# Kernel tuning notes

Measured on AMD Instinct MI355X. Metric: run time of the kernel, lower is better.

## Reference

```python
import jax, jax.numpy as jnp
import numpy as np

B, C, H, W = 2, 512, 64, 64
G = 32          # GroupNorm groups
EPS = 1e-6


def setup_inputs() -> dict:
    key = jax.random.key(0)
    ks = jax.random.split(key, 10)
    s = 1.0 / np.sqrt(C)
    return {
        "x": jax.random.normal(ks[0], (B, C, H, W), dtype=jnp.float32),
        "gn_w": jnp.ones((C,), jnp.float32),
        "gn_b": jnp.zeros((C,), jnp.float32),
        "wq": jax.random.normal(ks[1], (C, C), jnp.float32) * s,
        "bq": jnp.zeros((C,), jnp.float32),
        "wk": jax.random.normal(ks[2], (C, C), jnp.float32) * s,
        "bk": jnp.zeros((C,), jnp.float32),
        "wv": jax.random.normal(ks[3], (C, C), jnp.float32) * s,
        "bv": jnp.zeros((C,), jnp.float32),
        "wo": jax.random.normal(ks[4], (C, C), jnp.float32) * s,
        "bo": jnp.zeros((C,), jnp.float32),
    }


def reference(x, gn_w, gn_b, wq, bq, wk, bk, wv, bv, wo, bo):
    b, c, h, w = x.shape
    n = h * w
    # GroupNorm(32, eps=1e-6, affine)
    xg = x.reshape(b, G, c // G, h, w)
    mu = xg.mean(axis=(2, 3, 4), keepdims=True)
    var = ((xg - mu) ** 2).mean(axis=(2, 3, 4), keepdims=True)
    hn = ((xg - mu) * jax.lax.rsqrt(var + EPS)).reshape(b, c, h, w)
    hn = hn * gn_w[None, :, None, None] + gn_b[None, :, None, None]
    # 1x1 convs == per-pixel linear over channels; tokens: b n c
    hf = hn.reshape(b, c, n)
    q = jnp.einsum('oc,bcn->bno', wq, hf) + bq  # [b, n, c]
    k = jnp.einsum('oc,bcn->bno', wk, hf) + bk
    v = jnp.einsum('oc,bcn->bno', wv, hf) + bv
    scale = jnp.asarray(c, x.dtype) ** -0.5
    att = jax.nn.softmax(jnp.einsum('bic,bjc->bij', q, k) * scale, axis=-1)
    o = jnp.einsum('bij,bjc->bic', att, v)      # [b, n, c]
    out = jnp.einsum('oc,bnc->bno', wo, o) + bo # proj_out
    return x + out.transpose(0, 2, 1).reshape(b, c, h, w)
```

## Files before the change

kernel.cpp:

```cpp
#include <hip/hip_runtime.h>
#include <hip/hip_bf16.h>


typedef float f32x4 __attribute__((ext_vector_type(4)));
typedef __bf16 bf16x8 __attribute__((ext_vector_type(8)));

typedef const __attribute__((address_space(1))) unsigned char* gas_p;
typedef __attribute__((address_space(3))) unsigned char* las_p;

__device__ __forceinline__ void gload_lds16(const void* g, void* l) {
  __builtin_amdgcn_global_load_lds((gas_p)g, (las_p)l, 16, 0, 0);
}

__global__ __launch_bounds__(256) void prelude_k(
    const float* __restrict__ wq, const float* __restrict__ wk,
    const float* __restrict__ wv, const float* __restrict__ wo,
    __hip_bfloat16* __restrict__ wqkb, __hip_bfloat16* __restrict__ wvb,
    __hip_bfloat16* __restrict__ wob, const float* __restrict__ bq,
    const float* __restrict__ bk, float* __restrict__ bqk,
    const float* __restrict__ x, float* __restrict__ stats) {
  int bid = blockIdx.x;
  if (bid < 4096) {
    const float* src;
    __hip_bfloat16* dst;
    if (bid < 1024)      { src = wq; dst = wqkb; }
    else if (bid < 2048) { src = wk; dst = wqkb + 262144; }
    else if (bid < 3072) { src = wv; dst = wvb; }
    else                 { src = wo; dst = wob; }
    int i = (bid & 1023) * 256 + threadIdx.x;
    dst[i] = __float2bfloat16(src[i]);
    return;
  }
  if (bid < 4160) {
    int bg = bid - 4096;
    const float4* p = (const float4*)(x + (size_t)bg * 65536);
    float s = 0.f, s2 = 0.f;
    for (int i = threadIdx.x; i < 16384; i += 256) {
      float4 v = p[i];
      s  += v.x + v.y + v.z + v.w;
      s2 += v.x * v.x + v.y * v.y + v.z * v.z + v.w * v.w;
    }
#pragma unroll
    for (int off = 32; off > 0; off >>= 1) {
      s  += __shfl_xor(s, off);
      s2 += __shfl_xor(s2, off);
    }
    __shared__ float rs[4], rs2[4];
    int wid = threadIdx.x >> 6, lane = threadIdx.x & 63;
    if (lane == 0) { rs[wid] = s; rs2[wid] = s2; }
    __syncthreads();
    if (threadIdx.x == 0) {
      float S  = rs[0] + rs[1] + rs[2] + rs[3];
      float S2 = rs2[0] + rs2[1] + rs2[2] + rs2[3];
      float mean = S * (1.f / 65536.f);
      float var  = S2 * (1.f / 65536.f) - mean * mean;
      stats[bg * 2]     = mean;
      stats[bg * 2 + 1] = rsqrtf(var + 1e-6f);
    }
    return;
  }
  for (int j = threadIdx.x; j < 1024; j += 256)
    bqk[j] = (j < 512) ? bq[j] : bk[j - 512];
}

__global__ __launch_bounds__(256) void gn_apply_k(const float* __restrict__ x,
                                                  const float* __restrict__ stats,
                                                  const float* __restrict__ gw,
                                                  const float* __restrict__ gb,
                                                  __hip_bfloat16* __restrict__ hf) {
  int c0 = blockIdx.x * 64, n0 = blockIdx.y * 64, b = blockIdx.z;
  __shared__ float tile[64][65];
  int tid = threadIdx.x;
  int cl = tid >> 2, q = tid & 3;
  int c = c0 + cl;
  float mean = stats[(b * 32 + (c >> 4)) * 2];
  float rstd = stats[(b * 32 + (c >> 4)) * 2 + 1];
  float sc = rstd * gw[c];
  float sh = gb[c] - mean * sc;
  const float* xr = x + ((size_t)(b * 512 + c0 + cl)) * 4096 + n0 + q * 16;
#pragma unroll
  for (int j = 0; j < 4; j++) {
    float4 v = *(const float4*)(xr + 4 * j);
    int n = q * 16 + 4 * j;
    tile[cl][n]     = v.x * sc + sh;
    tile[cl][n + 1] = v.y * sc + sh;
    tile[cl][n + 2] = v.z * sc + sh;
    tile[cl][n + 3] = v.w * sc + sh;
  }
  __syncthreads();
  int nl = tid >> 2, ch = q * 16;
  bf16x8 o0, o1;
#pragma unroll
  for (int l = 0; l < 8; l++) {
    o0[l] = (__bf16)tile[ch + l][nl];
    o1[l] = (__bf16)tile[ch + 8 + l][nl];
  }
  __hip_bfloat16* op = hf + ((size_t)(b * 4096 + n0 + nl)) * 512 + c0 + ch;
  *(uint4*)op = *(uint4*)&o0;
  *(uint4*)(op + 8) = *(uint4*)&o1;
}

__global__ __launch_bounds__(256, 4) void qkv_k(
    const __hip_bfloat16* __restrict__ hf, const __hip_bfloat16* __restrict__ wqk,
    const __hip_bfloat16* __restrict__ wv, const float* __restrict__ bqk,
    const float* __restrict__ bv, __hip_bfloat16* __restrict__ qk,
    __hip_bfloat16* __restrict__ vT) {
  bool isV = blockIdx.x >= 8;
  int m0 = isV ? (blockIdx.x - 8) * 128 : blockIdx.y * 128;
  int n0 = isV ? blockIdx.y * 128 : blockIdx.x * 128;
  const __hip_bfloat16* A  = isV ? wv : hf;
  const __hip_bfloat16* Bm = isV ? hf : wqk;

  __shared__ __align__(16) unsigned char smem[34816];
  __hip_bfloat16* As  = (__hip_bfloat16*)smem;
  __hip_bfloat16* Bs  = As + 8192;
  __hip_bfloat16* epi = (__hip_bfloat16*)smem;

  int tid  = threadIdx.x;
  int wvx  = tid >> 6, lane = tid & 63;
  int wr   = (wvx >> 1) * 64, wc = (wvx & 1) * 64;
  int quad = lane >> 4, l16 = lane & 15;

  int srow = wvx * 32 + (lane >> 2);
  int scol = (lane & 3) * 8;
  const __hip_bfloat16* gA0 = A  + (size_t)(m0 + srow) * 512 + scol;
  const __hip_bfloat16* gA1 = gA0 + (size_t)16 * 512;
  const __hip_bfloat16* gB0 = Bm + (size_t)(n0 + srow) * 512 + scol;
  const __hip_bfloat16* gB1 = gB0 + (size_t)16 * 512;

  auto stage = [&](int kk, int bsel) {
    int lb = bsel * 4096 + wvx * 1024;
    gload_lds16(gA0 + kk, &As[lb]);
    gload_lds16(gA1 + kk, &As[lb + 512]);
    gload_lds16(gB0 + kk, &Bs[lb]);
    gload_lds16(gB1 + kk, &Bs[lb + 512]);
  };

  f32x4 acc[4][4] = {};
  stage(0, 0);
  for (int kt = 0; kt < 16; kt++) {
    __syncthreads();
    if (kt + 1 < 16) stage((kt + 1) << 5, (kt + 1) & 1);
    const __hip_bfloat16* Ab = &As[(kt & 1) * 4096];
    const __hip_bfloat16* Bb = &Bs[(kt & 1) * 4096];
    bf16x8 af[4], bfr[4];
#pragma unroll
    for (int i = 0; i < 4; i++)
      af[i] = *(const bf16x8*)&Ab[(wr + i * 16 + l16) * 32 + quad * 8];
#pragma unroll
    for (int j = 0; j < 4; j++)
      bfr[j] = *(const bf16x8*)&Bb[(wc + j * 16 + l16) * 32 + quad * 8];
#pragma unroll
    for (int i = 0; i < 4; i++)
#pragma unroll
      for (int j = 0; j < 4; j++)
        acc[i][j] = __builtin_amdgcn_mfma_f32_16x16x32_bf16(af[i], bfr[j],
                                                            acc[i][j], 0, 0, 0);
  }

  float bj[4], bm[4][4];
  if (!isV) {
#pragma unroll
    for (int j = 0; j < 4; j++) bj[j] = bqk[n0 + wc + j * 16 + l16];
  } else {
#pragma unroll
    for (int i = 0; i < 4; i++)
#pragma unroll
      for (int r = 0; r < 4; r++)
        bm[i][r] = bv[m0 + wr + i * 16 + quad * 4 + r];
  }
  __syncthreads();
#pragma unroll
  for (int i = 0; i < 4; i++)
#pragma unroll
    for (int j = 0; j < 4; j++)
#pragma unroll
      for (int r = 0; r < 4; r++) {
        int ml = wr + i * 16 + quad * 4 + r;
        int nl = wc + j * 16 + l16;
        float v = acc[i][j][r] + (isV ? bm[i][r] : bj[j]);
        epi[ml * 136 + nl] = __float2bfloat16(v);
      }
  __syncthreads();
  int mr = tid >> 1, h = tid & 1;
  const __hip_bfloat16* rowp = &epi[mr * 136 + h * 64];
  if (!isV) {
    __hip_bfloat16* o = qk + (size_t)(m0 + mr) * 1024 + n0 + h * 64;
#pragma unroll
    for (int c = 0; c < 8; c++)
      *(uint4*)(o + c * 8) = *(const uint4*)(rowp + c * 8);
  } else {
    int b = (n0 + h * 64) >> 12, t = (n0 + h * 64) & 4095;
    __hip_bfloat16* o = vT + ((size_t)(b * 512 + m0 + mr)) * 4096 + t;
#pragma unroll
    for (int c = 0; c < 8; c++)
      *(uint4*)(o + c * 8) = *(const uint4*)(rowp + c * 8);
  }
}

__global__ __launch_bounds__(256, 4) void qkexp_k(
    const __hip_bfloat16* __restrict__ A, const __hip_bfloat16* __restrict__ Bm,
    __hip_bfloat16* __restrict__ Cout, float* __restrict__ psums) {
  int bx = blockIdx.x, by = blockIdx.y, bb = blockIdx.z;
  const float scale = 0.044194173824159216f;
  A  += (size_t)bb * 4096 * 1024;
  Bm += (size_t)bb * 4096 * 1024 + 512;
  size_t cbase = (size_t)bb * 4096 * 4096;
  int m0 = by * 128, n0 = bx * 128;

  __shared__ __align__(16) unsigned char smem[33792];
  __hip_bfloat16* As  = (__hip_bfloat16*)smem;
  __hip_bfloat16* Bs  = As + 8192;
  float* psum2 = (float*)(smem + 32768);

  int tid  = threadIdx.x;
  int wv   = tid >> 6, lane = tid & 63;
  int wr   = (wv >> 1) * 64, wc = (wv & 1) * 64;
  int quad = lane >> 4, l16 = lane & 15;

  int srow = wv * 32 + (lane >> 2);
  int scol = (lane & 3) * 8;
  const __hip_bfloat16* gA0 = A  + (size_t)(m0 + srow) * 1024 + scol;
  const __hip_bfloat16* gA1 = gA0 + (size_t)16 * 1024;
  const __hip_bfloat16* gB0 = Bm + (size_t)(n0 + srow) * 1024 + scol;
  const __hip_bfloat16* gB1 = gB0 + (size_t)16 * 1024;

  auto stage = [&](int kk, int bsel) {
    int lb = bsel * 4096 + wv * 1024;
    gload_lds16(gA0 + kk, &As[lb]);
    gload_lds16(gA1 + kk, &As[lb + 512]);
    gload_lds16(gB0 + kk, &Bs[lb]);
    gload_lds16(gB1 + kk, &Bs[lb + 512]);
  };

  f32x4 acc[4][4] = {};
  stage(0, 0);
  for (int kt = 0; kt < 16; kt++) {
    __syncthreads();
    if (kt + 1 < 16) stage((kt + 1) << 5, (kt + 1) & 1);
    const __hip_bfloat16* Ab = &As[(kt & 1) * 4096];
    const __hip_bfloat16* Bb = &Bs[(kt & 1) * 4096];
    bf16x8 af[4], bfr[4];
#pragma unroll
    for (int i = 0; i < 4; i++)
      af[i] = *(const bf16x8*)&Ab[(wr + i * 16 + l16) * 32 + quad * 8];
#pragma unroll
    for (int j = 0; j < 4; j++)
      bfr[j] = *(const bf16x8*)&Bb[(wc + j * 16 + l16) * 32 + quad * 8];
#pragma unroll
    for (int i = 0; i < 4; i++)
#pragma unroll
      for (int j = 0; j < 4; j++)
        acc[i][j] = __builtin_amdgcn_mfma_f32_16x16x32_bf16(af[i], bfr[j],
                                                            acc[i][j], 0, 0, 0);
  }

  float s[4][4];
#pragma unroll
  for (int i = 0; i < 4; i++)
#pragma unroll
    for (int r = 0; r < 4; r++) s[i][r] = 0.f;
#pragma unroll
  for (int i = 0; i < 4; i++)
#pragma unroll
    for (int j = 0; j < 4; j++)
#pragma unroll
      for (int r = 0; r < 4; r++) {
        int m = m0 + wr + i * 16 + quad * 4 + r;
        int n = n0 + wc + j * 16 + l16;
        float v = __expf(acc[i][j][r] * scale);
        Cout[cbase + (size_t)m * 4096 + n] = __float2bfloat16(v);
        s[i][r] += v;
      }
#pragma unroll
  for (int off = 1; off < 16; off <<= 1)
#pragma unroll
    for (int i = 0; i < 4; i++)
#pragma unroll
      for (int r = 0; r < 4; r++) s[i][r] += __shfl_xor(s[i][r], off);
  if (l16 == 0) {
#pragma unroll
    for (int i = 0; i < 4; i++)
#pragma unroll
      for (int r = 0; r < 4; r++)
        psum2[(wv & 1) * 128 + wr + i * 16 + quad * 4 + r] = s[i][r];
  }
  __syncthreads();
  if (tid < 128)
    psums[(size_t)bx * 8192 + bb * 4096 + m0 + tid] =
        psum2[tid] + psum2[128 + tid];
}

__global__ __launch_bounds__(256, 2) void pv_k(
    const __hip_bfloat16* __restrict__ P, const __hip_bfloat16* __restrict__ vT,
    __hip_bfloat16* __restrict__ part) {
  int f = blockIdx.x;
  int xcd = f & 7, s = f >> 3;
  int bx = s & 3;
  int g = xcd + 8 * (s >> 2);
  int by = g & 31, bz = g >> 5;
  int bb = bz >> 1, ks = bz & 1;
  const __hip_bfloat16* A = P  + (size_t)bb * 4096 * 4096 + (size_t)ks * 2048;
  const __hip_bfloat16* B = vT + (size_t)bb * 512 * 4096 + (size_t)ks * 2048;
  size_t cbase = (size_t)bz * 4096 * 512;
  int m0 = by * 128, n0 = bx * 128;

  __shared__ __align__(16) unsigned char smem[65536];
  __hip_bfloat16* As  = (__hip_bfloat16*)smem;
  __hip_bfloat16* Bs  = (__hip_bfloat16*)(smem + 32768);
  __hip_bfloat16* epi = (__hip_bfloat16*)smem;

  int tid = threadIdx.x, wv = tid >> 6, lane = tid & 63;
  int wr = (wv >> 1) * 64, wc = (wv & 1) * 64;
  int quad = lane >> 4, l16 = lane & 15;

  int srow = wv * 32 + (lane >> 3);
  int scol = ((lane & 7) ^ (lane >> 3)) * 8;
  const __hip_bfloat16* gA = A + (size_t)(m0 + srow) * 4096 + scol;
  const __hip_bfloat16* gB = B + (size_t)(n0 + srow) * 4096 + scol;

  auto stage = [&](int kk, int bsel) {
    __hip_bfloat16* la = &As[bsel * 8192 + wv * 2048];
    __hip_bfloat16* lb = &Bs[bsel * 8192 + wv * 2048];
#pragma unroll
    for (int c = 0; c < 4; c++) {
      gload_lds16(gA + kk + (size_t)(c * 8) * 4096, la + c * 512);
      gload_lds16(gB + kk + (size_t)(c * 8) * 4096, lb + c * 512);
    }
  };

  f32x4 acc[4][4] = {};
  stage(0, 0);
  for (int kt = 0; kt < 32; kt++) {
    __syncthreads();
    if (kt + 1 < 32) stage((kt + 1) << 6, (kt + 1) & 1);
    const __hip_bfloat16* Ab = &As[(kt & 1) * 8192];
    const __hip_bfloat16* Bb = &Bs[(kt & 1) * 8192];
#pragma unroll
    for (int ksub = 0; ksub < 2; ksub++) {
      bf16x8 af[4], bfr[4];
#pragma unroll
      for (int i = 0; i < 4; i++) {
        int r = wr + i * 16 + l16;
        af[i] = *(const bf16x8*)&Ab[r * 64 + ((ksub * 4 + quad) ^ (r & 7)) * 8];
      }
#pragma unroll
      for (int j = 0; j < 4; j++) {
        int r = wc + j * 16 + l16;
        bfr[j] = *(const bf16x8*)&Bb[r * 64 + ((ksub * 4 + quad) ^ (r & 7)) * 8];
      }
#pragma unroll
      for (int i = 0; i < 4; i++)
#pragma unroll
        for (int j = 0; j < 4; j++)
          acc[i][j] = __builtin_amdgcn_mfma_f32_16x16x32_bf16(af[i], bfr[j],
                                                              acc[i][j], 0, 0, 0);
    }
  }

  __syncthreads();
#pragma unroll
  for (int i = 0; i < 4; i++)
#pragma unroll
    for (int j = 0; j < 4; j++)
#pragma unroll
      for (int r = 0; r < 4; r++)
        epi[(wr + i * 16 + quad * 4 + r) * 136 + wc + j * 16 + l16] =
            __float2bfloat16(acc[i][j][r]);
  __syncthreads();
  int mr = tid >> 1, h = tid & 1;
  const __hip_bfloat16* rowp = &epi[mr * 136 + h * 64];
  __hip_bfloat16* o = part + cbase + (size_t)(m0 + mr) * 512 + n0 + h * 64;
#pragma unroll
  for (int c = 0; c < 8; c++)
    *(uint4*)(o + c * 8) = *(const uint4*)(rowp + c * 8);
}

__global__ __launch_bounds__(256) void reduce_k(
    const __hip_bfloat16* __restrict__ part, const float* __restrict__ psums,
    __hip_bfloat16* __restrict__ obuf) {
  size_t i8 = (size_t)blockIdx.x * 256 + threadIdx.x;
  size_t perb = (size_t)4096 * 512 / 8;
  size_t b = i8 / perb, r = i8 - b * perb;
  int t = (int)(r >> 6);
  int lane = threadIdx.x & 63;
  float ps = psums[(size_t)(lane & 31) * 8192 + b * 4096 + t];
#pragma unroll
  for (int off = 1; off < 32; off <<= 1) ps += __shfl_xor(ps, off);
  float inv = 1.f / ps;
  float acc[8] = {};
#pragma unroll
  for (int ks = 0; ks < 2; ks++) {
    bf16x8 v = ((const bf16x8*)part)[(b * 2 + ks) * perb + r];
#pragma unroll
    for (int l = 0; l < 8; l++) acc[l] += (float)v[l];
  }
  bf16x8 o;
#pragma unroll
  for (int l = 0; l < 8; l++) o[l] = (__bf16)(acc[l] * inv);
  ((bf16x8*)obuf)[b * perb + r] = o;
}

__global__ __launch_bounds__(256, 2) void oproj_k(
    const __hip_bfloat16* __restrict__ Wo, const __hip_bfloat16* __restrict__ O,
    float* __restrict__ out, const float* __restrict__ bias,
    const float* __restrict__ resid) {
  int m0 = blockIdx.y * 64, n0 = blockIdx.x * 128, bb = blockIdx.z;
  O += (size_t)bb * 4096 * 512;
  size_t cbase = (size_t)bb * 512 * 4096;

  __shared__ __align__(16) unsigned char smem[24576];
  __hip_bfloat16* As  = (__hip_bfloat16*)smem;
  __hip_bfloat16* Bs  = As + 4096;
  __hip_bfloat16* epi = (__hip_bfloat16*)smem;

  int tid = threadIdx.x, wv = tid >> 6, lane = tid & 63;
  int wr = (wv >> 1) * 32, wc = (wv & 1) * 64;
  int quad = lane >> 4, l16 = lane & 15;

  int lr = lane >> 2, scol = (lane & 3) * 8;
  const __hip_bfloat16* gA  = Wo + (size_t)(m0 + wv * 16 + lr) * 512 + scol;
  const __hip_bfloat16* gB0 = O  + (size_t)(n0 + wv * 32 + lr) * 512 + scol;
  const __hip_bfloat16* gB1 = gB0 + (size_t)16 * 512;

  auto stage = [&](int kk, int bsel) {
    gload_lds16(gA + kk, &As[bsel * 2048 + wv * 512]);
    gload_lds16(gB0 + kk, &Bs[bsel * 4096 + wv * 1024]);
    gload_lds16(gB1 + kk, &Bs[bsel * 4096 + wv * 1024 + 512]);
  };

  f32x4 acc[2][4] = {};
  stage(0, 0);
  for (int kt = 0; kt < 16; kt++) {
    __syncthreads();
    if (kt + 1 < 16) stage((kt + 1) << 5, (kt + 1) & 1);
    const __hip_bfloat16* Ab = &As[(kt & 1) * 2048];
    const __hip_bfloat16* Bb = &Bs[(kt & 1) * 4096];
    bf16x8 af[2], bfr[4];
#pragma unroll
    for (int i = 0; i < 2; i++)
      af[i] = *(const bf16x8*)&Ab[(wr + i * 16 + l16) * 32 + quad * 8];
#pragma unroll
    for (int j = 0; j < 4; j++)
      bfr[j] = *(const bf16x8*)&Bb[(wc + j * 16 + l16) * 32 + quad * 8];
#pragma unroll
    for (int i = 0; i < 2; i++)
#pragma unroll
      for (int j = 0; j < 4; j++)
        acc[i][j] = __builtin_amdgcn_mfma_f32_16x16x32_bf16(af[i], bfr[j],
                                                            acc[i][j], 0, 0, 0);
  }

  float pre[2][4];
#pragma unroll
  for (int i = 0; i < 2; i++)
#pragma unroll
    for (int r = 0; r < 4; r++)
      pre[i][r] = bias[m0 + wr + i * 16 + quad * 4 + r];
  __syncthreads();
#pragma unroll
  for (int i = 0; i < 2; i++)
#pragma unroll
    for (int j = 0; j < 4; j++)
#pragma unroll
      for (int r = 0; r < 4; r++)
        epi[(wr + i * 16 + quad * 4 + r) * 136 + wc + j * 16 + l16] =
            __float2bfloat16(acc[i][j][r] + pre[i][r]);
  __syncthreads();
  int mr = tid >> 2, seg = tid & 3;
  const __hip_bfloat16* rowp = &epi[mr * 136 + seg * 32];
  size_t obase = cbase + (size_t)(m0 + mr) * 4096 + n0 + seg * 32;
#pragma unroll
  for (int c = 0; c < 4; c++) {
    bf16x8 val = *(const bf16x8*)(rowp + c * 8);
    size_t idx = obase + c * 8;
    float4 r0 = *(const float4*)&resid[idx];
    float4 r1 = *(const float4*)&resid[idx + 4];
    float4 o0, o1;
    o0.x = r0.x + (float)val[0]; o0.y = r0.y + (float)val[1];
    o0.z = r0.z + (float)val[2]; o0.w = r0.w + (float)val[3];
    o1.x = r1.x + (float)val[4]; o1.y = r1.y + (float)val[5];
    o1.z = r1.z + (float)val[6]; o1.w = r1.w + (float)val[7];
    *(float4*)&out[idx] = o0;
    *(float4*)&out[idx + 4] = o1;
  }
}

extern "C" void kernel_launch(void* const* d_in, const int* in_sizes, int n_in,
                              void* d_out, int out_size, void* d_ws,
                              size_t ws_size, hipStream_t stream) {
  const float* xp  = (const float*)d_in[0];
  const float* gwp = (const float*)d_in[1];
  const float* gbp = (const float*)d_in[2];
  const float* wqp = (const float*)d_in[3];
  const float* bqp = (const float*)d_in[4];
  const float* wkp = (const float*)d_in[5];
  const float* bkp = (const float*)d_in[6];
  const float* wvp = (const float*)d_in[7];
  const float* bvp = (const float*)d_in[8];
  const float* wop = (const float*)d_in[9];
  const float* bop = (const float*)d_in[10];
  float* outp = (float*)d_out;

  char* w = (char*)d_ws;
  size_t off = 0;
  auto alloc = [&](size_t bytes) {
    void* p = w + off;
    off += (bytes + 255) & ~(size_t)255;
    return p;
  };
  float* stats         = (float*)alloc(64 * 2 * sizeof(float));
  __hip_bfloat16* hf   = (__hip_bfloat16*)alloc((size_t)2 * 4096 * 512 * 2);
  __hip_bfloat16* wqkb = (__hip_bfloat16*)alloc((size_t)1024 * 512 * 2);
  __hip_bfloat16* wvb  = (__hip_bfloat16*)alloc((size_t)512 * 512 * 2);
  __hip_bfloat16* wob  = (__hip_bfloat16*)alloc((size_t)512 * 512 * 2);
  float* bqk           = (float*)alloc(1024 * sizeof(float));
  float* psums         = (float*)alloc((size_t)32 * 8192 * sizeof(float));
  __hip_bfloat16* qk   = (__hip_bfloat16*)alloc((size_t)2 * 4096 * 1024 * 2);
  __hip_bfloat16* vT   = (__hip_bfloat16*)alloc((size_t)2 * 512 * 4096 * 2);
  __hip_bfloat16* obuf = (__hip_bfloat16*)alloc((size_t)2 * 4096 * 512 * 2);
  __hip_bfloat16* part = (__hip_bfloat16*)alloc((size_t)4 * 4096 * 512 * 2);
  __hip_bfloat16* Sbuf = (__hip_bfloat16*)alloc((size_t)2 * 4096 * 4096 * 2);

  prelude_k<<<4161, 256, 0, stream>>>(wqp, wkp, wvp, wop, wqkb, wvb, wob,
                                      bqp, bkp, bqk, xp, stats);

  gn_apply_k<<<dim3(8, 64, 2), 256, 0, stream>>>(xp, stats, gwp, gbp, hf);

  qkv_k<<<dim3(12, 64, 1), 256, 0, stream>>>(hf, wqkb, wvb, bqk, bvp, qk, vT);

  qkexp_k<<<dim3(32, 32, 2), 256, 0, stream>>>(qk, qk, Sbuf, psums);

  pv_k<<<512, 256, 0, stream>>>(Sbuf, vT, part);

  reduce_k<<<2048, 256, 0, stream>>>(part, psums, obuf);

  oproj_k<<<dim3(32, 8, 2), 256, 0, stream>>>(wob, obuf, outp, bop, xp);
}
```

Baseline: 251.6 us.

## Fuse split-K partial reduction and softmax normalization into output projection

Removes the reduce_k kernel that summed the two split-K PV partials and divided by the softmax row sum. The output projection now loads both partial buffers, accumulates them with doubled MFMAs, and scales each token column by the inverse row sum in its epilogue. A small sum32_k kernel precomputes the row sums. This saves a full read/write pass over the intermediate attention output, at the cost of oproj reading twice the B data and using more LDS. The qkexp store loop is also reordered to hoist the row base address.

```diff
diff --git a/kernel.cpp b/kernel.cpp
--- a/kernel.cpp
+++ b/kernel.cpp
@@ -263,15 +263,16 @@
 #pragma unroll
   for (int i = 0; i < 4; i++)
 #pragma unroll
-    for (int j = 0; j < 4; j++)
-#pragma unroll
-      for (int r = 0; r < 4; r++) {
-        int m = m0 + wr + i * 16 + quad * 4 + r;
-        int n = n0 + wc + j * 16 + l16;
+    for (int r = 0; r < 4; r++) {
+      int m = m0 + wr + i * 16 + quad * 4 + r;
+      size_t rb = cbase + (size_t)m * 4096 + n0;
+#pragma unroll
+      for (int j = 0; j < 4; j++) {
         float v = __expf(acc[i][j][r] * scale);
-        Cout[cbase + (size_t)m * 4096 + n] = __float2bfloat16(v);
+        Cout[rb + wc + j * 16 + l16] = __float2bfloat16(v);
         s[i][r] += v;
       }
+    }
 #pragma unroll
   for (int off = 1; off < 16; off <<= 1)
 #pragma unroll
@@ -289,6 +290,15 @@
   if (tid < 128)
     psums[(size_t)bx * 8192 + bb * 4096 + m0 + tid] =
         psum2[tid] + psum2[128 + tid];
+}
+
+__global__ __launch_bounds__(256) void sum32_k(const float* __restrict__ psums,
+                                               float* __restrict__ rowsumf) {
+  int i = blockIdx.x * 256 + threadIdx.x;
+  float s = 0.f;
+#pragma unroll
+  for (int j = 0; j < 32; j++) s += psums[(size_t)j * 8192 + i];
+  rowsumf[i] = s;
 }
 
 __global__ __launch_bounds__(256, 2) void pv_k(
@@ -376,42 +386,19 @@
     *(uint4*)(o + c * 8) = *(const uint4*)(rowp + c * 8);
 }
 
-__global__ __launch_bounds__(256) void reduce_k(
-    const __hip_bfloat16* __restrict__ part, const float* __restrict__ psums,
-    __hip_bfloat16* __restrict__ obuf) {
-  size_t i8 = (size_t)blockIdx.x * 256 + threadIdx.x;
-  size_t perb = (size_t)4096 * 512 / 8;
-  size_t b = i8 / perb, r = i8 - b * perb;
-  int t = (int)(r >> 6);
-  int lane = threadIdx.x & 63;
-  float ps = psums[(size_t)(lane & 31) * 8192 + b * 4096 + t];
-#pragma unroll
-  for (int off = 1; off < 32; off <<= 1) ps += __shfl_xor(ps, off);
-  float inv = 1.f / ps;
-  float acc[8] = {};
-#pragma unroll
-  for (int ks = 0; ks < 2; ks++) {
-    bf16x8 v = ((const bf16x8*)part)[(b * 2 + ks) * perb + r];
-#pragma unroll
-    for (int l = 0; l < 8; l++) acc[l] += (float)v[l];
-  }
-  bf16x8 o;
-#pragma unroll
-  for (int l = 0; l < 8; l++) o[l] = (__bf16)(acc[l] * inv);
-  ((bf16x8*)obuf)[b * perb + r] = o;
-}
-
 __global__ __launch_bounds__(256, 2) void oproj_k(
-    const __hip_bfloat16* __restrict__ Wo, const __hip_bfloat16* __restrict__ O,
+    const __hip_bfloat16* __restrict__ Wo, const __hip_bfloat16* __restrict__ part,
     float* __restrict__ out, const float* __restrict__ bias,
-    const float* __restrict__ resid) {
+    const float* __restrict__ resid, const float* __restrict__ rowsumf) {
   int m0 = blockIdx.y * 64, n0 = blockIdx.x * 128, bb = blockIdx.z;
-  O += (size_t)bb * 4096 * 512;
+  const __hip_bfloat16* P0 = part + (size_t)(bb * 2) * 4096 * 512;
+  const __hip_bfloat16* P1 = P0 + (size_t)4096 * 512;
   size_t cbase = (size_t)bb * 512 * 4096;
 
-  __shared__ __align__(16) unsigned char smem[24576];
+  __shared__ __align__(16) unsigned char smem[40960];
   __hip_bfloat16* As  = (__hip_bfloat16*)smem;
-  __hip_bfloat16* Bs  = As + 4096;
+  __hip_bfloat16* B0s = As + 4096;
+  __hip_bfloat16* B1s = B0s + 8192;
   __hip_bfloat16* epi = (__hip_bfloat16*)smem;
 
   int tid = threadIdx.x, wv = tid >> 6, lane = tid & 63;
@@ -419,14 +406,18 @@
   int quad = lane >> 4, l16 = lane & 15;
 
   int lr = lane >> 2, scol = (lane & 3) * 8;
-  const __hip_bfloat16* gA  = Wo + (size_t)(m0 + wv * 16 + lr) * 512 + scol;
-  const __hip_bfloat16* gB0 = O  + (size_t)(n0 + wv * 32 + lr) * 512 + scol;
-  const __hip_bfloat16* gB1 = gB0 + (size_t)16 * 512;
+  const __hip_bfloat16* gA   = Wo + (size_t)(m0 + wv * 16 + lr) * 512 + scol;
+  const __hip_bfloat16* gB0a = P0 + (size_t)(n0 + wv * 32 + lr) * 512 + scol;
+  const __hip_bfloat16* gB0b = gB0a + (size_t)16 * 512;
+  const __hip_bfloat16* gB1a = P1 + (size_t)(n0 + wv * 32 + lr) * 512 + scol;
+  const __hip_bfloat16* gB1b = gB1a + (size_t)16 * 512;
 
   auto stage = [&](int kk, int bsel) {
-    gload_lds16(gA + kk, &As[bsel * 2048 + wv * 512]);
-    gload_lds16(gB0 + kk, &Bs[bsel * 4096 + wv * 1024]);
-    gload_lds16(gB1 + kk, &Bs[bsel * 4096 + wv * 1024 + 512]);
+    gload_lds16(gA + kk,   &As[bsel * 2048 + wv * 512]);
+    gload_lds16(gB0a + kk, &B0s[bsel * 4096 + wv * 1024]);
+    gload_lds16(gB0b + kk, &B0s[bsel * 4096 + wv * 1024 + 512]);
+    gload_lds16(gB1a + kk, &B1s[bsel * 4096 + wv * 1024]);
+    gload_lds16(gB1b + kk, &B1s[bsel * 4096 + wv * 1024 + 512]);
   };
 
   f32x4 acc[2][4] = {};
@@ -434,29 +425,38 @@
   for (int kt = 0; kt < 16; kt++) {
     __syncthreads();
     if (kt + 1 < 16) stage((kt + 1) << 5, (kt + 1) & 1);
-    const __hip_bfloat16* Ab = &As[(kt & 1) * 2048];
-    const __hip_bfloat16* Bb = &Bs[(kt & 1) * 4096];
-    bf16x8 af[2], bfr[4];
+    const __hip_bfloat16* Ab  = &As[(kt & 1) * 2048];
+    const __hip_bfloat16* Bb0 = &B0s[(kt & 1) * 4096];
+    const __hip_bfloat16* Bb1 = &B1s[(kt & 1) * 4096];
+    bf16x8 af[2], b0[4], b1[4];
 #pragma unroll
     for (int i = 0; i < 2; i++)
       af[i] = *(const bf16x8*)&Ab[(wr + i * 16 + l16) * 32 + quad * 8];
 #pragma unroll
-    for (int j = 0; j < 4; j++)
-      bfr[j] = *(const bf16x8*)&Bb[(wc + j * 16 + l16) * 32 + quad * 8];
+    for (int j = 0; j < 4; j++) {
+      b0[j] = *(const bf16x8*)&Bb0[(wc + j * 16 + l16) * 32 + quad * 8];
+      b1[j] = *(const bf16x8*)&Bb1[(wc + j * 16 + l16) * 32 + quad * 8];
+    }
 #pragma unroll
     for (int i = 0; i < 2; i++)
 #pragma unroll
-      for (int j = 0; j < 4; j++)
-        acc[i][j] = __builtin_amdgcn_mfma_f32_16x16x32_bf16(af[i], bfr[j],
+      for (int j = 0; j < 4; j++) {
+        acc[i][j] = __builtin_amdgcn_mfma_f32_16x16x32_bf16(af[i], b0[j],
                                                             acc[i][j], 0, 0, 0);
-  }
-
-  float pre[2][4];
+        acc[i][j] = __builtin_amdgcn_mfma_f32_16x16x32_bf16(af[i], b1[j],
+                                                            acc[i][j], 0, 0, 0);
+      }
+  }
+
+  float pre[2][4], invj[4];
 #pragma unroll
   for (int i = 0; i < 2; i++)
 #pragma unroll
     for (int r = 0; r < 4; r++)
       pre[i][r] = bias[m0 + wr + i * 16 + quad * 4 + r];
+#pragma unroll
+  for (int j = 0; j < 4; j++)
+    invj[j] = 1.f / rowsumf[bb * 4096 + n0 + wc + j * 16 + l16];
   __syncthreads();
 #pragma unroll
   for (int i = 0; i < 2; i++)
@@ -465,7 +465,7 @@
 #pragma unroll
       for (int r = 0; r < 4; r++)
         epi[(wr + i * 16 + quad * 4 + r) * 136 + wc + j * 16 + l16] =
-            __float2bfloat16(acc[i][j][r] + pre[i][r]);
+            __float2bfloat16(acc[i][j][r] * invj[j] + pre[i][r]);
   __syncthreads();
   int mr = tid >> 2, seg = tid & 3;
   const __hip_bfloat16* rowp = &epi[mr * 136 + seg * 32];
@@ -516,9 +516,9 @@
   __hip_bfloat16* wob  = (__hip_bfloat16*)alloc((size_t)512 * 512 * 2);
   float* bqk           = (float*)alloc(1024 * sizeof(float));
   float* psums         = (float*)alloc((size_t)32 * 8192 * sizeof(float));
+  float* rowsumf       = (float*)alloc(8192 * sizeof(float));
   __hip_bfloat16* qk   = (__hip_bfloat16*)alloc((size_t)2 * 4096 * 1024 * 2);
   __hip_bfloat16* vT   = (__hip_bfloat16*)alloc((size_t)2 * 512 * 4096 * 2);
-  __hip_bfloat16* obuf = (__hip_bfloat16*)alloc((size_t)2 * 4096 * 512 * 2);
   __hip_bfloat16* part = (__hip_bfloat16*)alloc((size_t)4 * 4096 * 512 * 2);
   __hip_bfloat16* Sbuf = (__hip_bfloat16*)alloc((size_t)2 * 4096 * 4096 * 2);
 
@@ -531,9 +531,10 @@
 
   qkexp_k<<<dim3(32, 32, 2), 256, 0, stream>>>(qk, qk, Sbuf, psums);
 
+  sum32_k<<<32, 256, 0, stream>>>(psums, rowsumf);
+
   pv_k<<<512, 256, 0, stream>>>(Sbuf, vT, part);
 
-  reduce_k<<<2048, 256, 0, stream>>>(part, psums, obuf);
-
-  oproj_k<<<dim3(32, 8, 2), 256, 0, stream>>>(wob, obuf, outp, bop, xp);
-}
+  oproj_k<<<dim3(32, 8, 2), 256, 0, stream>>>(wob, part, outp, bop, xp,
+                                              rowsumf);
+}
```

Measured after the change: 255.6 us. No clear change (+1.6%).
